# Optimization experiments

Measured on AMD Instinct MI355X. Metric: run time of the kernel, lower is better.

The kernel has to match this reference:

```python
import jax, jax.numpy as jnp
import numpy as np

N = 4096      # num nodes
E = 131072    # num edges
D = 128       # embed dim (in=out)
HID = 16      # kan hidden dim
G, K = 4, 3   # KAN grid_size / spline_order (GCN + FFN kans)
GA, KA = 2, 1 # attention KANLinear grid_size / spline_order
H, HD = 8, 16 # heads, head_dim

def make_grid(in_f, g, k):
    h = 2.0 / g
    pts = (np.arange(-k, g + k + 1) * h - 1.0).astype(np.float32)  # [g+2k+1]
    return jnp.asarray(np.tile(pts[None, :], (in_f, 1)))            # [in_f, g+2k+1]

GRID_D = make_grid(D, G, K)
GRID_H = make_grid(HID, G, K)
GRID_A = make_grid(D, GA, KA)

def b_splines(x, grid, k):
    # x: [n, in] -> B-spline bases [n, in, g+k] via Cox-de-Boor recursion
    x = x[:, :, None]
    g = grid[None]
    bases = ((x >= g[..., :-1]) & (x < g[..., 1:])).astype(x.dtype)
    for j in range(1, k + 1):
        bases = ((x - g[..., :-(j + 1)]) / (g[..., j:-1] - g[..., :-(j + 1)]) * bases[..., :-1]
                 + (g[..., j + 1:] - x) / (g[..., j + 1:] - g[..., 1:-j]) * bases[..., 1:])
    return bases

def kan_lin(x, bw, sw, grid, k, use_silu):
    base = jax.nn.silu(x) if use_silu else x
    return base @ bw.T + jnp.einsum('nig,oig->no', b_splines(x, grid, k), sw)

def ekan2(x, bw1, sw1, bw2, sw2):
    # eKAN with layers_hidden=[D, HID, D], SiLU base activation
    h = kan_lin(x, bw1, sw1, GRID_D, K, True)
    return kan_lin(h, bw2, sw2, GRID_H, K, True)

def layer_norm(h, s, b):
    m = jnp.mean(h, axis=-1, keepdims=True)
    v = jnp.var(h, axis=-1, keepdims=True)
    return (h - m) * jax.lax.rsqrt(v + 1e-5) * s + b

def setup_inputs() -> dict:
    key = jax.random.key(0)
    ks = jax.random.split(key, 20)
    r = lambda i, shape: jax.random.normal(ks[i], shape, jnp.float32) * 0.1
    return dict(
        x=jax.random.normal(ks[0], (N, D), jnp.float32),
        edge_index=jax.random.randint(ks[1], (2, E), 0, N),
        gcn_bw1=r(2, (HID, D)), gcn_sw1=r(3, (HID, D, G + K)),
        gcn_bw2=r(4, (D, HID)), gcn_sw2=r(5, (D, HID, G + K)),
        q_bw=r(6, (D, D)), q_sw=r(7, (D, D, GA + KA)),
        k_bw=r(8, (D, D)), k_sw=r(9, (D, D, GA + KA)),
        v_bw=r(10, (D, D)), v_sw=r(11, (D, D, GA + KA)),
        ffn_bw1=r(12, (HID, D)), ffn_sw1=r(13, (HID, D, G + K)),
        ffn_bw2=r(14, (D, HID)), ffn_sw2=r(15, (D, HID, G + K)),
        ln1_s=jnp.ones(D), ln1_b=jnp.zeros(D),
        ln2_s=jnp.ones(D), ln2_b=jnp.zeros(D),
        ln3_s=jnp.ones(D), ln3_b=jnp.zeros(D),
    )

def reference(x, edge_index, gcn_bw1, gcn_sw1, gcn_bw2, gcn_sw2,
              q_bw, q_sw, k_bw, k_sw, v_bw, v_sw,
              ffn_bw1, ffn_sw1, ffn_bw2, ffn_sw2,
              ln1_s, ln1_b, ln2_s, ln2_b, ln3_s, ln3_b):
    n = x.shape[0]
    # ---- local GCN-KAN branch: KAN(A_hat x) ----
    loops = jnp.arange(n)
    row = jnp.concatenate([edge_index[0], loops])  # sources (+ self-loops)
    col = jnp.concatenate([edge_index[1], loops])  # targets
    w = jnp.ones(row.shape[0], x.dtype)
    deg = jax.ops.segment_sum(w, row, num_segments=n)
    dis = jnp.where(deg > 0, deg ** -0.5, 0.0)
    norm = dis[row] * w * dis[col]
    agg = jax.ops.segment_sum(norm[:, None] * x[row], col, num_segments=n)  # [n, D]
    h_local = ekan2(agg, gcn_bw1, gcn_sw1, gcn_bw2, gcn_sw2)
    h_local = layer_norm(x + h_local, ln1_s, ln1_b)
    # ---- global KAN multi-head attention branch ----
    Q = kan_lin(x, q_bw, q_sw, GRID_A, KA, False).reshape(n, H, HD)
    Kv = kan_lin(x, k_bw, k_sw, GRID_A, KA, False).reshape(n, H, HD)
    V = kan_lin(x, v_bw, v_sw, GRID_A, KA, False).reshape(n, H, HD)
    scores = jnp.einsum('nhd,mhd->hnm', Q, Kv) / np.sqrt(HD)  # [H, n, n]
    attn = jax.nn.softmax(scores, axis=-1)
    h_attn = jnp.einsum('hnm,mhd->nhd', attn, V).reshape(n, D)
    h_attn = layer_norm(x + h_attn, ln2_s, ln2_b)
    # ---- combine + KAN feed-forward ----
    h = h_local + h_attn
    out = layer_norm(h + ekan2(h, ffn_bw1, ffn_sw1, ffn_bw2, ffn_sw2), ln3_s, ln3_b)
    return out
```

## Files before the change

### kernel.cpp

```cpp
#include <hip/hip_runtime.h>

typedef unsigned short u16;
typedef unsigned int u32;

#define D_ 128
#define HID_ 16
#define NH_ 8
#define HD_ 16
#define PSTRIDE 17

#define WE_W1G 0
#define WE_W2G 16384
#define WE_W1F 32768
#define WE_W2F 49152
#define WE_TOTAL 65536

#define KROW 24
#define VROW 136
#define PROW 40
#define HROW 136

#define QSCALE 0.3606737602222409f

typedef __attribute__((ext_vector_type(8))) short bfrag;
typedef __attribute__((ext_vector_type(4))) float ffrag;

#if defined(__has_builtin)
#if __has_builtin(__builtin_amdgcn_exp2f)
#define EXP2F(x) __builtin_amdgcn_exp2f(x)
#endif
#endif
#ifndef EXP2F
#define EXP2F(x) exp2f(x)
#endif


__device__ __forceinline__ float bf2f(u16 u) {
    union { u32 i; float f; } v; v.i = ((u32)u) << 16; return v.f;
}
__device__ __forceinline__ u16 f2bf(float f) {
    u32 x = __float_as_uint(f);
    u32 r = (x + 0x7fffu + ((x >> 16) & 1u)) >> 16;
    return (u16)r;
}
__device__ __forceinline__ float rdf(const void* p, int i, bool bf) {
    return bf ? bf2f(((const u16*)p)[i]) : ((const float*)p)[i];
}

__device__ __forceinline__ u32 probe_stat(const u16* p) {
    for (int i = 0; i < 128; i++) {
        u16 u = p[i];
        int e = (u >> 7) & 0xFF;
        int m = u & 0x7F;
        bool zero = (e == 0) && (m == 0);
        bool sane = zero || (e >= 97 && e <= 147);
        if (!sane) return 0u;
    }
    return 1u;
}

__global__ __launch_bounds__(256) void k_detect(const void* x,
                         const void* gbw1, const void* gsw1, const void* gbw2, const void* gsw2,
                         const void* qbw, const void* qsw, const void* kbw, const void* ksw,
                         const void* vbw, const void* vsw,
                         const void* fbw1, const void* fsw1, const void* fbw2, const void* fsw2,
                         const void* l1s, const void* l1b, const void* l2s, const void* l2b,
                         const void* l3s, const void* l3b,
                         u32* flags, int* __restrict__ cnt3, int N) {
    int t = threadIdx.x;
    const void* ptrs[21] = {x, gbw1, gsw1, gbw2, gsw2, qbw, qsw, kbw, ksw, vbw, vsw,
                            fbw1, fsw1, fbw2, fsw2, l1s, l1b, l2s, l2b, l3s, l3b};
    if (t < 21) {
        u32 f = 0;
        if (t == 15 || t == 17 || t == 19) {
            f = (((const u32*)ptrs[t])[0] != 0x3F800000u) ? 1u : 0u;
        } else if (t == 16 || t == 18 || t == 20) {
            f = 0;
        } else {
            f = probe_stat((const u16*)ptrs[t]);
        }
        flags[t] = f;
    }
    __syncthreads();
    if (t == 16 || t == 18 || t == 20) flags[t] = flags[t - 1];
    int tot = 3 * N;
    for (int i = t; i < tot; i += 256) cnt3[i] = 0;
}

__device__ __forceinline__ float cub_seg(float s) {
    if (s < 0.0f || s >= 4.0f) return 0.0f;
    if (s < 1.0f) return s * s * s * (1.0f / 6.0f);
    if (s < 2.0f) { float r = s - 1.0f; return (1.0f + 3.0f * r + 3.0f * r * r - 3.0f * r * r * r) * (1.0f / 6.0f); }
    if (s < 3.0f) { float r = s - 2.0f; return (4.0f - 6.0f * r * r + 3.0f * r * r * r) * (1.0f / 6.0f); }
    float q = 4.0f - s; return q * q * q * (1.0f / 6.0f);
}
__device__ __forceinline__ float lin_seg(float s) {
    if (s < 0.0f || s >= 2.0f) return 0.0f;
    return (s < 1.0f) ? s : (2.0f - s);
}

__device__ __forceinline__ float bsum(float v, float* tmp) {
#pragma unroll
    for (int off = 1; off < 64; off <<= 1) v += __shfl_xor(v, off, 64);
    __syncthreads();
    if ((threadIdx.x & 63) == 0) tmp[threadIdx.x >> 6] = v;
    __syncthreads();
    return tmp[0] + tmp[1];
}

__device__ __forceinline__ uint4 feat8(float a) {
    float si = a / (1.0f + __expf(-a));
    float u = (a + 2.5f) * 2.0f;
    float b0 = cub_seg(u), b1 = cub_seg(u - 1.0f), b2 = cub_seg(u - 2.0f), b3 = cub_seg(u - 3.0f);
    float b4 = cub_seg(u - 4.0f), b5 = cub_seg(u - 5.0f), b6 = cub_seg(u - 6.0f);
    uint4 r;
    r.x = (u32)f2bf(si) | ((u32)f2bf(b0) << 16);
    r.y = (u32)f2bf(b1) | ((u32)f2bf(b2) << 16);
    r.z = (u32)f2bf(b3) | ((u32)f2bf(b4) << 16);
    r.w = (u32)f2bf(b5) | ((u32)f2bf(b6) << 16);
    return r;
}

__global__ __launch_bounds__(256) void k_setup(const void* __restrict__ x,
        const void* l1s, const void* l1b, const void* l2s,
        const void* l2b, const void* l3s, const void* l3b,
        const void* gbw1, const void* gsw1, const void* gbw2, const void* gsw2,
        const void* fbw1, const void* fsw1, const void* fbw2, const void* fsw2,
        const void* qbw, const void* qsw, const void* kbw, const void* ksw,
        const void* vbw, const void* vsw,
        const int* __restrict__ ei,
        const u32* __restrict__ flags,
        float* __restrict__ xin, float* __restrict__ lnp,
        u16* __restrict__ F,
        u16* __restrict__ Web, u16* __restrict__ Wb,
        int* __restrict__ cnt, int* __restrict__ degi,
        int N, int E) {
    int b = blockIdx.x;
    int convB = ((N * D_ + 768) + 255) >> 8;
    if (b < convB) {
        int i = b * 256 + threadIdx.x;
        if (i < N * D_) {
            float xv = rdf(x, i, flags[0] != 0);
            xin[i] = xv;
            float u = xv + 2.0f;
            u32 lo = (u32)f2bf(xv) | ((u32)f2bf(lin_seg(u)) << 16);
            u32 hi = (u32)f2bf(lin_seg(u - 1.0f)) | ((u32)f2bf(lin_seg(u - 2.0f)) << 16);
            ((uint2*)F)[i] = make_uint2(lo, hi);
        } else if (i < N * D_ + 768) {
            int j = i - N * D_;
            int sel = j >> 7, k = j & 127;
            const void* p = sel == 0 ? l1s : sel == 1 ? l1b : sel == 2 ? l2s
                         : sel == 3 ? l2b : sel == 4 ? l3s : l3b;
            lnp[j] = rdf(p, k, flags[15 + sel] != 0);
        }
    } else if (b < convB + 224) {
        int t = (b - convB) * 256 + threadIdx.x;
        if (t < 8192) {
            int seg = t >> 11, i = t & 2047;
            const void* bw = seg == 0 ? gbw1 : seg == 1 ? gbw2 : seg == 2 ? fbw1 : fbw2;
            const void* sw = seg == 0 ? gsw1 : seg == 1 ? gsw2 : seg == 2 ? fsw1 : fsw2;
            int fb = seg == 0 ? 1 : seg == 1 ? 3 : seg == 2 ? 11 : 13;
            bool bwbf = flags[fb] != 0, swbf = flags[fb + 1] != 0;
            u16* dst = Web + (size_t)seg * 16384 + (size_t)i * 8;
            dst[0] = f2bf(rdf(bw, i, bwbf));
#pragma unroll
            for (int g = 0; g < 7; g++) dst[1 + g] = f2bf(rdf(sw, i * 7 + g, swbf));
        } else if (t < 8192 + 49152) {
            int uu = t - 8192;
            int seg = uu >> 14, i = uu & 16383;
            const void* bw = seg == 0 ? qbw : seg == 1 ? kbw : vbw;
            const void* sw = seg == 0 ? qsw : seg == 1 ? ksw : vsw;
            int fb = 5 + seg * 2;
            bool bwbf = flags[fb] != 0, swbf = flags[fb + 1] != 0;
            float sc = (seg == 0) ? QSCALE : 1.0f;
            u16* dst = Wb + (size_t)seg * 65536 + (size_t)i * 4;
            dst[0] = f2bf(rdf(bw, i, bwbf) * sc);
#pragma unroll
            for (int g = 0; g < 3; g++) dst[1 + g] = f2bf(rdf(sw, i * 3 + g, swbf) * sc);
        }
    } else {
        int e = (b - convB - 224) * 256 + threadIdx.x;
        if (e < E) {
            atomicAdd(&degi[ei[e]], 1);
            atomicAdd(&cnt[ei[E + e]], 1);
        }
    }
}

__global__ __launch_bounds__(1024) void k_scan(const int* __restrict__ cnt,
                                               const int* __restrict__ degi,
                                               int* __restrict__ rowptr,
                                               float* __restrict__ dis, int N) {
    __shared__ int ws[16];
    int t = threadIdx.x;
    int base = t * 4;
    int a[4];
#pragma unroll
    for (int k = 0; k < 4; k++) a[k] = (base + k < N) ? cnt[base + k] : 0;
    int loc = a[0] + a[1] + a[2] + a[3];
    int pre = loc;
#pragma unroll
    for (int off = 1; off < 64; off <<= 1) {
        int v = __shfl_up(pre, off, 64);
        if ((t & 63) >= off) pre += v;
    }
    if ((t & 63) == 63) ws[t >> 6] = pre;
    __syncthreads();
    if (t < 64) {
        int v = (t < 16) ? ws[t] : 0;
#pragma unroll
        for (int off = 1; off < 16; off <<= 1) {
            int u = __shfl_up(v, off, 64);
            if (t >= off) v += u;
        }
        if (t < 16) ws[t] = v;
    }
    __syncthreads();
    int ex = pre - loc + ((t >= 64) ? ws[(t >> 6) - 1] : 0);
    int run = ex;
#pragma unroll
    for (int k = 0; k < 4; k++) {
        if (base + k < N) rowptr[base + k] = run;
        run += a[k];
    }
    if (t == 1023) rowptr[N] = ws[15];
#pragma unroll
    for (int k = 0; k < 4; k++)
        if (base + k < N) dis[base + k] = rsqrtf((float)degi[base + k] + 1.0f);
}

__global__ void k_fill(const int* __restrict__ ei, const int* __restrict__ rowptr,
                       int* __restrict__ fill, int* __restrict__ elist, int E) {
    int e = blockIdx.x * 256 + threadIdx.x;
    if (e < E) {
        int r = ei[e], c = ei[E + e];
        int pos = rowptr[c] + atomicAdd(&fill[c], 1);
        elist[pos] = r;
    }
}

__global__ __launch_bounds__(128) void k_gcn(const int* __restrict__ rowptr,
        const int* __restrict__ elist, const float* __restrict__ dis,
        const float* __restrict__ xin, u16* __restrict__ Afeat) {
    int c = blockIdx.x, t = threadIdx.x;
    __shared__ int ids[128];
    __shared__ float wsh[128];
    int beg = rowptr[c], end = rowptr[c + 1];
    float acc = 0.0f, acc2 = 0.0f;
    for (int j0 = beg; j0 < end; j0 += 128) {
        int cc = min(128, end - j0);
        __syncthreads();
        if (t < cc) {
            int rr = elist[j0 + t];
            ids[t] = rr;
            wsh[t] = dis[rr];
        }
        __syncthreads();
        int j = 0;
        for (; j + 2 <= cc; j += 2) {
            acc  += wsh[j]     * xin[(size_t)ids[j] * D_ + t];
            acc2 += wsh[j + 1] * xin[(size_t)ids[j + 1] * D_ + t];
        }
        if (j < cc) acc += wsh[j] * xin[(size_t)ids[j] * D_ + t];
    }
    float dc = dis[c];
    float a = dc * (acc + acc2 + dc * xin[(size_t)c * D_ + t]);
    ((uint4*)Afeat)[(size_t)c * D_ + t] = feat8(a);
}

__global__ __launch_bounds__(64) void k_ekan_mm(const u16* __restrict__ A,
        const u16* __restrict__ W1b, const u16* __restrict__ W2b,
        const float* __restrict__ resid,
        const float* __restrict__ lns, const float* __restrict__ lnb,
        void* __restrict__ outp, const u32* __restrict__ flags, int fin, int N) {
    __shared__ u16 hfL[16 * HROW];
    int mt = blockIdx.x;
    int lane = threadIdx.x, quad = lane >> 4, l15 = lane & 15;
    const u16* ar = A + (size_t)(mt * 16 + l15) * 1024 + quad * 8;
    const u16* br = W1b + (size_t)l15 * 1024 + quad * 8;
    ffrag acc = {0, 0, 0, 0};
#pragma unroll
    for (int ks = 0; ks < 1024; ks += 32) {
        bfrag af = *(const bfrag*)(ar + ks);
        bfrag bf = *(const bfrag*)(br + ks);
        acc = __builtin_amdgcn_mfma_f32_16x16x32_bf16(af, bf, acc, 0, 0, 0);
    }
#define G1EPI(RR, COMP) { \
    uint4 fv = feat8(acc.COMP); \
    *(uint4*)(&hfL[(quad * 4 + RR) * HROW + l15 * 8]) = fv; }
    G1EPI(0, x) G1EPI(1, y) G1EPI(2, z) G1EPI(3, w)
#undef G1EPI
    __asm__ volatile("s_waitcnt lgkmcnt(0)" ::: "memory");
    __builtin_amdgcn_wave_barrier();
    const u16* b0 = W2b + (size_t)l15 * 128 + quad * 8;
    ffrag a0 = {0,0,0,0}, a1 = {0,0,0,0}, a2 = {0,0,0,0}, a3 = {0,0,0,0};
    ffrag a4 = {0,0,0,0}, a5 = {0,0,0,0}, a6 = {0,0,0,0}, a7 = {0,0,0,0};
#pragma unroll
    for (int ks = 0; ks < 128; ks += 32) {
        bfrag af = *(const bfrag*)(&hfL[l15 * HROW + quad * 8 + ks]);
        a0 = __builtin_amdgcn_mfma_f32_16x16x32_bf16(af, *(const bfrag*)(b0 + 0 * 2048 + ks), a0, 0, 0, 0);
        a1 = __builtin_amdgcn_mfma_f32_16x16x32_bf16(af, *(const bfrag*)(b0 + 1 * 2048 + ks), a1, 0, 0, 0);
        a2 = __builtin_amdgcn_mfma_f32_16x16x32_bf16(af, *(const bfrag*)(b0 + 2 * 2048 + ks), a2, 0, 0, 0);
        a3 = __builtin_amdgcn_mfma_f32_16x16x32_bf16(af, *(const bfrag*)(b0 + 3 * 2048 + ks), a3, 0, 0, 0);
        a4 = __builtin_amdgcn_mfma_f32_16x16x32_bf16(af, *(const bfrag*)(b0 + 4 * 2048 + ks), a4, 0, 0, 0);
        a5 = __builtin_amdgcn_mfma_f32_16x16x32_bf16(af, *(const bfrag*)(b0 + 5 * 2048 + ks), a5, 0, 0, 0);
        a6 = __builtin_amdgcn_mfma_f32_16x16x32_bf16(af, *(const bfrag*)(b0 + 6 * 2048 + ks), a6, 0, 0, 0);
        a7 = __builtin_amdgcn_mfma_f32_16x16x32_bf16(af, *(const bfrag*)(b0 + 7 * 2048 + ks), a7, 0, 0, 0);
    }
    float ls0 = lns[l15],       lb0 = lnb[l15];
    float ls1 = lns[16 + l15],  lb1 = lnb[16 + l15];
    float ls2 = lns[32 + l15],  lb2 = lnb[32 + l15];
    float ls3 = lns[48 + l15],  lb3 = lnb[48 + l15];
    float ls4 = lns[64 + l15],  lb4 = lnb[64 + l15];
    float ls5 = lns[80 + l15],  lb5 = lnb[80 + l15];
    float ls6 = lns[96 + l15],  lb6 = lnb[96 + l15];
    float ls7 = lns[112 + l15], lb7 = lnb[112 + l15];
    bool bfo = (fin != 0) && (flags[0] != 0);
#define G2EPI(RR, COMP) { \
    int node = mt * 16 + quad * 4 + RR; \
    const float* rr_ = resid + (size_t)node * 128 + l15; \
    float v0 = a0.COMP + rr_[0];   float v1 = a1.COMP + rr_[16]; \
    float v2 = a2.COMP + rr_[32];  float v3 = a3.COMP + rr_[48]; \
    float v4 = a4.COMP + rr_[64];  float v5 = a5.COMP + rr_[80]; \
    float v6 = a6.COMP + rr_[96];  float v7 = a7.COMP + rr_[112]; \
    float s1 = ((v0 + v1) + (v2 + v3)) + ((v4 + v5) + (v6 + v7)); \
    float s2 = ((v0*v0 + v1*v1) + (v2*v2 + v3*v3)) + ((v4*v4 + v5*v5) + (v6*v6 + v7*v7)); \
    s1 += __shfl_xor(s1, 1, 64); s2 += __shfl_xor(s2, 1, 64); \
    s1 += __shfl_xor(s1, 2, 64); s2 += __shfl_xor(s2, 2, 64); \
    s1 += __shfl_xor(s1, 4, 64); s2 += __shfl_xor(s2, 4, 64); \
    s1 += __shfl_xor(s1, 8, 64); s2 += __shfl_xor(s2, 8, 64); \
    float mean = s1 * 0.0078125f; \
    float var = s2 * 0.0078125f - mean * mean; \
    float rs = rsqrtf(var + 1e-5f); \
    float y0 = (v0 - mean) * rs * ls0 + lb0; float y1 = (v1 - mean) * rs * ls1 + lb1; \
    float y2 = (v2 - mean) * rs * ls2 + lb2; float y3 = (v3 - mean) * rs * ls3 + lb3; \
    float y4 = (v4 - mean) * rs * ls4 + lb4; float y5 = (v5 - mean) * rs * ls5 + lb5; \
    float y6 = (v6 - mean) * rs * ls6 + lb6; float y7 = (v7 - mean) * rs * ls7 + lb7; \
    if (bfo) { \
        u16* ob = (u16*)outp + (size_t)node * 128 + l15; \
        ob[0] = f2bf(y0); ob[16] = f2bf(y1); ob[32] = f2bf(y2); ob[48] = f2bf(y3); \
        ob[64] = f2bf(y4); ob[80] = f2bf(y5); ob[96] = f2bf(y6); ob[112] = f2bf(y7); \
    } else { \
        float* ob = (float*)outp + (size_t)node * 128 + l15; \
        ob[0] = y0; ob[16] = y1; ob[32] = y2; ob[48] = y3; \
        ob[64] = y4; ob[80] = y5; ob[96] = y6; ob[112] = y7; \
    } }
    G2EPI(0, x) G2EPI(1, y) G2EPI(2, z) G2EPI(3, w)
#undef G2EPI
}

#define QKV_STORE(ACC, TL) { \
    int col = cg * 48 + (TL) * 16 + l15; \
    int mat = col >> 7, idx = col & 127; \
    u16* dstb = (mat == 0) ? Qb : (mat == 1) ? Kb : Vb; \
    size_t base = (size_t)(idx >> 4) * N * HD_ + (size_t)(idx & 15); \
    dstb[base + (size_t)(rowb + 0) * HD_] = f2bf(ACC.x); \
    dstb[base + (size_t)(rowb + 1) * HD_] = f2bf(ACC.y); \
    dstb[base + (size_t)(rowb + 2) * HD_] = f2bf(ACC.z); \
    dstb[base + (size_t)(rowb + 3) * HD_] = f2bf(ACC.w); \
}

__global__ __launch_bounds__(64) void k_qkv5(const u16* __restrict__ F,
        const u16* __restrict__ Wb,
        u16* __restrict__ Qb, u16* __restrict__ Kb, u16* __restrict__ Vb, int N) {
    int mt = blockIdx.x, cg = blockIdx.y;
    int lane = threadIdx.x, quad = lane >> 4, l15 = lane & 15;
    const u16* arow = F + (size_t)(mt * 16 + l15) * 512 + quad * 8;
    const u16* b0r = Wb + (size_t)(cg * 48 + l15) * 512 + quad * 8;
    const u16* b1r = b0r + 16 * 512;
    const u16* b2r = b0r + 32 * 512;
    ffrag a0 = {0, 0, 0, 0}, a1 = {0, 0, 0, 0}, a2 = {0, 0, 0, 0};
#pragma unroll
    for (int ks = 0; ks < 512; ks += 32) {
        bfrag af = *(const bfrag*)(arow + ks);
        bfrag bf0 = *(const bfrag*)(b0r + ks);
        bfrag bf1 = *(const bfrag*)(b1r + ks);
        bfrag bf2 = *(const bfrag*)(b2r + ks);
        a0 = __builtin_amdgcn_mfma_f32_16x16x32_bf16(af, bf0, a0, 0, 0, 0);
        a1 = __builtin_amdgcn_mfma_f32_16x16x32_bf16(af, bf1, a1, 0, 0, 0);
        a2 = __builtin_amdgcn_mfma_f32_16x16x32_bf16(af, bf2, a2, 0, 0, 0);
    }
    int rowb = mt * 16 + quad * 4;
    QKV_STORE(a0, 0)
    QKV_STORE(a1, 1)
    QKV_STORE(a2, 2)
}

#define ATTN_SCORE(QF, LACC, PBT) { \
    ffrag zz = {0.0f, 0.0f, 0.0f, 0.0f}; \
    ffrag s0 = __builtin_amdgcn_mfma_f32_16x16x32_bf16(QF, kf0, zz, 0, 0, 0); \
    ffrag s1 = __builtin_amdgcn_mfma_f32_16x16x32_bf16(QF, kf1, zz, 0, 0, 0); \
    float a0 = EXP2F(s0.x), a1 = EXP2F(s0.y), a2 = EXP2F(s0.z), a3 = EXP2F(s0.w); \
    float b0 = EXP2F(s1.x), b1 = EXP2F(s1.y), b2 = EXP2F(s1.z), b3 = EXP2F(s1.w); \
    LACC.x += a0 + b0; LACC.y += a1 + b1; LACC.z += a2 + b2; LACC.w += a3 + b3; \
    u32* pw = (u32*)PBT; \
    pw[(quad * 4 + 0) * (PROW / 2) + l15] = (__float_as_uint(a0) >> 16) | (__float_as_uint(b0) & 0xFFFF0000u); \
    pw[(quad * 4 + 1) * (PROW / 2) + l15] = (__float_as_uint(a1) >> 16) | (__float_as_uint(b1) & 0xFFFF0000u); \
    pw[(quad * 4 + 2) * (PROW / 2) + l15] = (__float_as_uint(a2) >> 16) | (__float_as_uint(b2) & 0xFFFF0000u); \
    pw[(quad * 4 + 3) * (PROW / 2) + l15] = (__float_as_uint(a3) >> 16) | (__float_as_uint(b3) & 0xFFFF0000u); \
}

#define ATTN_PV(OACC, PBT) { \
    bfrag pf = *(const bfrag*)(&PBT[l15 * PROW + quad * 8]); \
    OACC = __builtin_amdgcn_mfma_f32_16x16x32_bf16(pf, vf, OACC, 0, 0, 0); \
}

#define STORE_TILE(OACC, LACC, TL) { \
    int q0 = qtb + (TL) * 16 + quad * 4; \
    float* pp; \
    pp = part + ((size_t)(h * N + q0 + 0) * SPLIT + s) * PSTRIDE; \
    pp[1 + l15] = OACC.x; if (l15 == 0) pp[0] = LACC.x; \
    pp = part + ((size_t)(h * N + q0 + 1) * SPLIT + s) * PSTRIDE; \
    pp[1 + l15] = OACC.y; if (l15 == 0) pp[0] = LACC.y; \
    pp = part + ((size_t)(h * N + q0 + 2) * SPLIT + s) * PSTRIDE; \
    pp[1 + l15] = OACC.z; if (l15 == 0) pp[0] = LACC.z; \
    pp = part + ((size_t)(h * N + q0 + 3) * SPLIT + s) * PSTRIDE; \
    pp[1 + l15] = OACC.w; if (l15 == 0) pp[0] = LACC.w; \
}

__global__ __launch_bounds__(256) void k_attn9(const u16* __restrict__ Qb,
        const u16* __restrict__ Kb, const u16* __restrict__ Vb,
        float* __restrict__ part, int N, int SPLIT) {
    int s = blockIdx.x, qb = blockIdx.y, h = blockIdx.z;
    int t = threadIdx.x;
    int w = t >> 6, lane = t & 63, quad = lane >> 4, l15 = lane & 15;
    __shared__ u16 ldsK[128 * KROW + 16];
    __shared__ u16 ldsVt[16 * VROW];
    __shared__ u16 ldsP[4][4][16 * PROW];

    const u16* qrow = Qb + (size_t)h * N * HD_;
    const u16* krow = Kb + (size_t)h * N * HD_;
    const u16* vrow = Vb + (size_t)h * N * HD_;

    for (int i = t; i < (128 * KROW + 16) / 2; i += 256) ((u32*)ldsK)[i] = 0;

    int qtb = qb * 256 + w * 64;
    bfrag qz = {0, 0, 0, 0, 0, 0, 0, 0};
    bfrag qf0 = qz, qf1 = qz, qf2 = qz, qf3 = qz;
    if (quad < 2) {
        qf0 = *(const bfrag*)(qrow + (size_t)(qtb + 0 * 16 + l15) * HD_ + quad * 8);
        qf1 = *(const bfrag*)(qrow + (size_t)(qtb + 1 * 16 + l15) * HD_ + quad * 8);
        qf2 = *(const bfrag*)(qrow + (size_t)(qtb + 2 * 16 + l15) * HD_ + quad * 8);
        qf3 = *(const bfrag*)(qrow + (size_t)(qtb + 3 * 16 + l15) * HD_ + quad * 8);
    }

    ffrag o0 = {0, 0, 0, 0}, o1 = {0, 0, 0, 0}, o2 = {0, 0, 0, 0}, o3 = {0, 0, 0, 0};
    ffrag L0 = {0, 0, 0, 0}, L1 = {0, 0, 0, 0}, L2 = {0, 0, 0, 0}, L3 = {0, 0, 0, 0};
    u16* pb0 = &ldsP[w][0][0];
    u16* pb1 = &ldsP[w][1][0];
    u16* pb2 = &ldsP[w][2][0];
    u16* pb3 = &ldsP[w][3][0];

    int keys = N / SPLIT;
    int kstart0 = s * keys;
    for (int kst = 0; kst < keys; kst += 128) {
        int kg = kstart0 + kst;
        __syncthreads();
        if (t < 128) {
            const uint4* src = (const uint4*)(krow + (size_t)(kg + t) * HD_);
            uint4 a = src[0], b = src[1];
            *(uint4*)(&ldsK[t * KROW]) = a;
            *(uint4*)(&ldsK[t * KROW + 8]) = b;
        } else {
            int key = t - 128;
            const uint4* src = (const uint4*)(vrow + (size_t)(kg + key) * HD_);
            uint4 a = src[0], b = src[1];
            ldsVt[0 * VROW + key] = (u16)(a.x);  ldsVt[1 * VROW + key] = (u16)(a.x >> 16);
            ldsVt[2 * VROW + key] = (u16)(a.y);  ldsVt[3 * VROW + key] = (u16)(a.y >> 16);
            ldsVt[4 * VROW + key] = (u16)(a.z);  ldsVt[5 * VROW + key] = (u16)(a.z >> 16);
            ldsVt[6 * VROW + key] = (u16)(a.w);  ldsVt[7 * VROW + key] = (u16)(a.w >> 16);
            ldsVt[8 * VROW + key] = (u16)(b.x);  ldsVt[9 * VROW + key] = (u16)(b.x >> 16);
            ldsVt[10 * VROW + key] = (u16)(b.y); ldsVt[11 * VROW + key] = (u16)(b.y >> 16);
            ldsVt[12 * VROW + key] = (u16)(b.z); ldsVt[13 * VROW + key] = (u16)(b.z >> 16);
            ldsVt[14 * VROW + key] = (u16)(b.w); ldsVt[15 * VROW + key] = (u16)(b.w >> 16);
        }
        __syncthreads();
#pragma unroll
        for (int koff = 0; koff < 128; koff += 32) {
            bfrag kf0 = *(const bfrag*)(&ldsK[(koff + 2 * l15) * KROW + quad * 8]);
            bfrag kf1 = *(const bfrag*)(&ldsK[(koff + 2 * l15 + 1) * KROW + quad * 8]);
            bfrag vf = *(const bfrag*)(&ldsVt[l15 * VROW + koff + quad * 8]);
            ATTN_SCORE(qf0, L0, pb0)
            ATTN_SCORE(qf1, L1, pb1)
            ATTN_SCORE(qf2, L2, pb2)
            ATTN_SCORE(qf3, L3, pb3)
            __asm__ volatile("s_waitcnt lgkmcnt(0)" ::: "memory");
            ATTN_PV(o0, pb0)
            ATTN_PV(o1, pb1)
            ATTN_PV(o2, pb2)
            ATTN_PV(o3, pb3)
        }
    }

#pragma unroll
    for (int off = 1; off < 16; off <<= 1) {
        L0.x += __shfl_xor(L0.x, off, 64); L0.y += __shfl_xor(L0.y, off, 64);
        L0.z += __shfl_xor(L0.z, off, 64); L0.w += __shfl_xor(L0.w, off, 64);
        L1.x += __shfl_xor(L1.x, off, 64); L1.y += __shfl_xor(L1.y, off, 64);
        L1.z += __shfl_xor(L1.z, off, 64); L1.w += __shfl_xor(L1.w, off, 64);
        L2.x += __shfl_xor(L2.x, off, 64); L2.y += __shfl_xor(L2.y, off, 64);
        L2.z += __shfl_xor(L2.z, off, 64); L2.w += __shfl_xor(L2.w, off, 64);
        L3.x += __shfl_xor(L3.x, off, 64); L3.y += __shfl_xor(L3.y, off, 64);
        L3.z += __shfl_xor(L3.z, off, 64); L3.w += __shfl_xor(L3.w, off, 64);
    }
    STORE_TILE(o0, L0, 0)
    STORE_TILE(o1, L1, 1)
    STORE_TILE(o2, L2, 2)
    STORE_TILE(o3, L3, 3)
}

__global__ __launch_bounds__(128) void k_comb(const float* __restrict__ part,
        const float* __restrict__ xin, const float* __restrict__ hl,
        const float* __restrict__ lnp, float* __restrict__ hv,
        u16* __restrict__ Afeat, int N, int SPLIT) {
    int n = blockIdx.x, t = threadIdx.x;
    __shared__ float red[128];
    int h = t >> 4, d = t & 15;
    float L = 0.0f, O = 0.0f;
    for (int ss = 0; ss < SPLIT; ss++) {
        const float* ps = part + ((size_t)(h * N + n) * SPLIT + ss) * PSTRIDE;
        L += ps[0];
        O += ps[1 + d];
    }
    float ha = O / L;
    float r = xin[(size_t)n * D_ + t] + ha;
    float mean = bsum(r, red) * (1.0f / 128.0f);
    float c = r - mean;
    float var = bsum(c * c, red) * (1.0f / 128.0f);
    float y2 = c * rsqrtf(var + 1e-5f) * lnp[256 + t] + lnp[384 + t];
    float hvv = hl[(size_t)n * D_ + t] + y2;
    hv[(size_t)n * D_ + t] = hvv;
    ((uint4*)Afeat)[(size_t)n * D_ + t] = feat8(hvv);
}

extern "C" void kernel_launch(void* const* d_in, const int* in_sizes, int n_in,
                              void* d_out, int out_size, void* d_ws, size_t ws_size,
                              hipStream_t stream) {
    const void* x = d_in[0];
    const int* ei = (const int*)d_in[1];
    const void* gbw1 = d_in[2];
    const void* gsw1 = d_in[3];
    const void* gbw2 = d_in[4];
    const void* gsw2 = d_in[5];
    const void* qbw = d_in[6];
    const void* qsw = d_in[7];
    const void* kbw = d_in[8];
    const void* ksw = d_in[9];
    const void* vbw = d_in[10];
    const void* vsw = d_in[11];
    const void* fbw1 = d_in[12];
    const void* fsw1 = d_in[13];
    const void* fbw2 = d_in[14];
    const void* fsw2 = d_in[15];
    const void* ln1s = d_in[16];
    const void* ln1b = d_in[17];
    const void* ln2s = d_in[18];
    const void* ln2b = d_in[19];
    const void* ln3s = d_in[20];
    const void* ln3b = d_in[21];

    const int N = in_sizes[0] / D_;
    const int E = in_sizes[1] / 2;
    const size_t ND = (size_t)N * D_;

    float* wf = (float*)d_ws;
    u32* flags = (u32*)wf;
    float* lnp = wf + 32;
    float* dis = wf + 800;
    float* xin = dis + N;
    float* hl  = xin + ND;
    float* hv  = hl + ND;
    u16* Web = (u16*)(hv + ND);
    u16* Wb  = Web + WE_TOTAL;
    u16* F   = Wb + 196608;
    u16* Qb  = F + (size_t)N * 512;
    u16* Kb  = Qb + ND;
    u16* Vb  = Kb + ND;
    u16* Afeat = Vb + ND;
    int* cnt    = (int*)(Afeat + (size_t)N * 1024);
    int* fill   = cnt + N;
    int* degi   = fill + N;
    int* rowptr = degi + N;
    int* elist  = rowptr + N + 1;
    float* part = (float*)(elist + E);

    size_t baseBytes = (size_t)((char*)part - (char*)d_ws);
    int SPLIT = 8;
    if (baseBytes + (size_t)NH_ * N * 8 * PSTRIDE * 4 > ws_size) SPLIT = 4;
    if (baseBytes + (size_t)NH_ * N * 4 * PSTRIDE * 4 > ws_size) SPLIT = 2;

    int convB = ((N * D_ + 768) + 255) >> 8;
    int countB = (E + 255) / 256;

    k_detect<<<1, 256, 0, stream>>>(x, gbw1, gsw1, gbw2, gsw2, qbw, qsw, kbw, ksw,
                                    vbw, vsw, fbw1, fsw1, fbw2, fsw2,
                                    ln1s, ln1b, ln2s, ln2b, ln3s, ln3b, flags, cnt, N);
    k_setup<<<convB + 224 + countB, 256, 0, stream>>>(
        x, ln1s, ln1b, ln2s, ln2b, ln3s, ln3b,
        gbw1, gsw1, gbw2, gsw2, fbw1, fsw1, fbw2, fsw2,
        qbw, qsw, kbw, ksw, vbw, vsw,
        ei, flags, xin, lnp, F, Web, Wb, cnt, degi, N, E);
    k_scan<<<1, 1024, 0, stream>>>(cnt, degi, rowptr, dis, N);
    k_fill<<<countB, 256, 0, stream>>>(ei, rowptr, fill, elist, E);
    k_gcn<<<N, 128, 0, stream>>>(rowptr, elist, dis, xin, Afeat);
    k_ekan_mm<<<N / 16, 64, 0, stream>>>(Afeat, Web + WE_W1G, Web + WE_W2G, xin,
                                         lnp + 0, lnp + 128, hl, flags, 0, N);
    k_qkv5<<<dim3(N / 16, 8), 64, 0, stream>>>(F, Wb, Qb, Kb, Vb, N);
    k_attn9<<<dim3(SPLIT, N / 256, NH_), 256, 0, stream>>>(Qb, Kb, Vb, part, N, SPLIT);
    k_comb<<<N, 128, 0, stream>>>(part, xin, hl, lnp, hv, Afeat, N, SPLIT);
    k_ekan_mm<<<N / 16, 64, 0, stream>>>(Afeat, Web + WE_W1F, Web + WE_W2F, hv,
                                         lnp + 512, lnp + 640, d_out, flags, 1, N);
}
```

Measured before the change: 241.7 us.

## Fuse GCN aggregation and combine stages with eKAN matmuls via shared-memory features

```diff
diff --git a/kernel.cpp b/kernel.cpp
--- a/kernel.cpp
+++ b/kernel.cpp
@@ -19,6 +19,8 @@
 #define VROW 136
 #define PROW 40
 #define HROW 136
+#define AROW 1032
+#define HVROW 132
 
 #define QSCALE 0.3606737602222409f
 
@@ -97,15 +99,6 @@
 __device__ __forceinline__ float lin_seg(float s) {
     if (s < 0.0f || s >= 2.0f) return 0.0f;
     return (s < 1.0f) ? s : (2.0f - s);
-}
-
-__device__ __forceinline__ float bsum(float v, float* tmp) {
-#pragma unroll
-    for (int off = 1; off < 64; off <<= 1) v += __shfl_xor(v, off, 64);
-    __syncthreads();
-    if ((threadIdx.x & 63) == 0) tmp[threadIdx.x >> 6] = v;
-    __syncthreads();
-    return tmp[0] + tmp[1];
 }
 
 __device__ __forceinline__ uint4 feat8(float a) {
@@ -239,114 +232,135 @@
     }
 }
 
-__global__ __launch_bounds__(128) void k_gcn(const int* __restrict__ rowptr,
-        const int* __restrict__ elist, const float* __restrict__ dis,
-        const float* __restrict__ xin, u16* __restrict__ Afeat) {
-    int c = blockIdx.x, t = threadIdx.x;
-    __shared__ int ids[128];
-    __shared__ float wsh[128];
-    int beg = rowptr[c], end = rowptr[c + 1];
-    float acc = 0.0f, acc2 = 0.0f;
-    for (int j0 = beg; j0 < end; j0 += 128) {
-        int cc = min(128, end - j0);
-        __syncthreads();
-        if (t < cc) {
-            int rr = elist[j0 + t];
-            ids[t] = rr;
-            wsh[t] = dis[rr];
-        }
-        __syncthreads();
-        int j = 0;
-        for (; j + 2 <= cc; j += 2) {
-            acc  += wsh[j]     * xin[(size_t)ids[j] * D_ + t];
-            acc2 += wsh[j + 1] * xin[(size_t)ids[j + 1] * D_ + t];
-        }
-        if (j < cc) acc += wsh[j] * xin[(size_t)ids[j] * D_ + t];
-    }
-    float dc = dis[c];
-    float a = dc * (acc + acc2 + dc * xin[(size_t)c * D_ + t]);
-    ((uint4*)Afeat)[(size_t)c * D_ + t] = feat8(a);
-}
-
-__global__ __launch_bounds__(64) void k_ekan_mm(const u16* __restrict__ A,
-        const u16* __restrict__ W1b, const u16* __restrict__ W2b,
-        const float* __restrict__ resid,
-        const float* __restrict__ lns, const float* __restrict__ lnb,
-        void* __restrict__ outp, const u32* __restrict__ flags, int fin, int N) {
-    __shared__ u16 hfL[16 * HROW];
-    int mt = blockIdx.x;
-    int lane = threadIdx.x, quad = lane >> 4, l15 = lane & 15;
-    const u16* ar = A + (size_t)(mt * 16 + l15) * 1024 + quad * 8;
-    const u16* br = W1b + (size_t)l15 * 1024 + quad * 8;
-    ffrag acc = {0, 0, 0, 0};
-#pragma unroll
-    for (int ks = 0; ks < 1024; ks += 32) {
-        bfrag af = *(const bfrag*)(ar + ks);
-        bfrag bf = *(const bfrag*)(br + ks);
-        acc = __builtin_amdgcn_mfma_f32_16x16x32_bf16(af, bf, acc, 0, 0, 0);
-    }
-#define G1EPI(RR, COMP) { \
-    uint4 fv = feat8(acc.COMP); \
-    *(uint4*)(&hfL[(quad * 4 + RR) * HROW + l15 * 8]) = fv; }
-    G1EPI(0, x) G1EPI(1, y) G1EPI(2, z) G1EPI(3, w)
-#undef G1EPI
-    __asm__ volatile("s_waitcnt lgkmcnt(0)" ::: "memory");
-    __builtin_amdgcn_wave_barrier();
-    const u16* b0 = W2b + (size_t)l15 * 128 + quad * 8;
-    ffrag a0 = {0,0,0,0}, a1 = {0,0,0,0}, a2 = {0,0,0,0}, a3 = {0,0,0,0};
-    ffrag a4 = {0,0,0,0}, a5 = {0,0,0,0}, a6 = {0,0,0,0}, a7 = {0,0,0,0};
-#pragma unroll
-    for (int ks = 0; ks < 128; ks += 32) {
-        bfrag af = *(const bfrag*)(&hfL[l15 * HROW + quad * 8 + ks]);
-        a0 = __builtin_amdgcn_mfma_f32_16x16x32_bf16(af, *(const bfrag*)(b0 + 0 * 2048 + ks), a0, 0, 0, 0);
-        a1 = __builtin_amdgcn_mfma_f32_16x16x32_bf16(af, *(const bfrag*)(b0 + 1 * 2048 + ks), a1, 0, 0, 0);
-        a2 = __builtin_amdgcn_mfma_f32_16x16x32_bf16(af, *(const bfrag*)(b0 + 2 * 2048 + ks), a2, 0, 0, 0);
-        a3 = __builtin_amdgcn_mfma_f32_16x16x32_bf16(af, *(const bfrag*)(b0 + 3 * 2048 + ks), a3, 0, 0, 0);
-        a4 = __builtin_amdgcn_mfma_f32_16x16x32_bf16(af, *(const bfrag*)(b0 + 4 * 2048 + ks), a4, 0, 0, 0);
-        a5 = __builtin_amdgcn_mfma_f32_16x16x32_bf16(af, *(const bfrag*)(b0 + 5 * 2048 + ks), a5, 0, 0, 0);
-        a6 = __builtin_amdgcn_mfma_f32_16x16x32_bf16(af, *(const bfrag*)(b0 + 6 * 2048 + ks), a6, 0, 0, 0);
-        a7 = __builtin_amdgcn_mfma_f32_16x16x32_bf16(af, *(const bfrag*)(b0 + 7 * 2048 + ks), a7, 0, 0, 0);
-    }
-    float ls0 = lns[l15],       lb0 = lnb[l15];
-    float ls1 = lns[16 + l15],  lb1 = lnb[16 + l15];
-    float ls2 = lns[32 + l15],  lb2 = lnb[32 + l15];
-    float ls3 = lns[48 + l15],  lb3 = lnb[48 + l15];
-    float ls4 = lns[64 + l15],  lb4 = lnb[64 + l15];
-    float ls5 = lns[80 + l15],  lb5 = lnb[80 + l15];
-    float ls6 = lns[96 + l15],  lb6 = lnb[96 + l15];
-    float ls7 = lns[112 + l15], lb7 = lnb[112 + l15];
-    bool bfo = (fin != 0) && (flags[0] != 0);
-#define G2EPI(RR, COMP) { \
-    int node = mt * 16 + quad * 4 + RR; \
-    const float* rr_ = resid + (size_t)node * 128 + l15; \
-    float v0 = a0.COMP + rr_[0];   float v1 = a1.COMP + rr_[16]; \
-    float v2 = a2.COMP + rr_[32];  float v3 = a3.COMP + rr_[48]; \
-    float v4 = a4.COMP + rr_[64];  float v5 = a5.COMP + rr_[80]; \
-    float v6 = a6.COMP + rr_[96];  float v7 = a7.COMP + rr_[112]; \
-    float s1 = ((v0 + v1) + (v2 + v3)) + ((v4 + v5) + (v6 + v7)); \
-    float s2 = ((v0*v0 + v1*v1) + (v2*v2 + v3*v3)) + ((v4*v4 + v5*v5) + (v6*v6 + v7*v7)); \
+#define EKAN_G1(W1B) \
+    if (ww == 0) { \
+        const u16* ar = hfA + (size_t)l15 * AROW + quad * 8; \
+        const u16* br = (W1B) + (size_t)l15 * 1024 + quad * 8; \
+        ffrag c0 = {0,0,0,0}, c1 = {0,0,0,0}, c2 = {0,0,0,0}, c3 = {0,0,0,0}; \
+        for (int ks = 0; ks < 256; ks += 32) { \
+            c0 = __builtin_amdgcn_mfma_f32_16x16x32_bf16(*(const bfrag*)(ar + ks),       *(const bfrag*)(br + ks),       c0, 0, 0, 0); \
+            c1 = __builtin_amdgcn_mfma_f32_16x16x32_bf16(*(const bfrag*)(ar + 256 + ks), *(const bfrag*)(br + 256 + ks), c1, 0, 0, 0); \
+            c2 = __builtin_amdgcn_mfma_f32_16x16x32_bf16(*(const bfrag*)(ar + 512 + ks), *(const bfrag*)(br + 512 + ks), c2, 0, 0, 0); \
+            c3 = __builtin_amdgcn_mfma_f32_16x16x32_bf16(*(const bfrag*)(ar + 768 + ks), *(const bfrag*)(br + 768 + ks), c3, 0, 0, 0); \
+        } \
+        float e0 = (c0.x + c1.x) + (c2.x + c3.x); \
+        float e1 = (c0.y + c1.y) + (c2.y + c3.y); \
+        float e2 = (c0.z + c1.z) + (c2.z + c3.z); \
+        float e3 = (c0.w + c1.w) + (c2.w + c3.w); \
+        { uint4 fv = feat8(e0); *(uint4*)(&hfL[(quad * 4 + 0) * HROW + l15 * 8]) = fv; } \
+        { uint4 fv = feat8(e1); *(uint4*)(&hfL[(quad * 4 + 1) * HROW + l15 * 8]) = fv; } \
+        { uint4 fv = feat8(e2); *(uint4*)(&hfL[(quad * 4 + 2) * HROW + l15 * 8]) = fv; } \
+        { uint4 fv = feat8(e3); *(uint4*)(&hfL[(quad * 4 + 3) * HROW + l15 * 8]) = fv; } \
+    }
+
+#define EK_TGET(RR, COMP, V0, V1, RES0EXPR, RES1EXPR) { \
+    int row = quad * 4 + RR; \
+    float r0 = (RES0EXPR); \
+    float r1 = (RES1EXPR); \
+    V0 = a0.COMP + r0; V1 = a1.COMP + r1; \
+    float s1 = V0 + V1, s2 = V0 * V0 + V1 * V1; \
     s1 += __shfl_xor(s1, 1, 64); s2 += __shfl_xor(s2, 1, 64); \
     s1 += __shfl_xor(s1, 2, 64); s2 += __shfl_xor(s2, 2, 64); \
     s1 += __shfl_xor(s1, 4, 64); s2 += __shfl_xor(s2, 4, 64); \
     s1 += __shfl_xor(s1, 8, 64); s2 += __shfl_xor(s2, 8, 64); \
+    if (l15 == 0) { redS[ww * 16 + row] = s1; redS[64 + ww * 16 + row] = s2; } }
+
+#define EK_TOUT(RR, V0, V1, OUTP, BFO) { \
+    int row = quad * 4 + RR; \
+    float s1 = (redS[row] + redS[16 + row]) + (redS[32 + row] + redS[48 + row]); \
+    float s2 = (redS[64 + row] + redS[80 + row]) + (redS[96 + row] + redS[112 + row]); \
     float mean = s1 * 0.0078125f; \
     float var = s2 * 0.0078125f - mean * mean; \
     float rs = rsqrtf(var + 1e-5f); \
-    float y0 = (v0 - mean) * rs * ls0 + lb0; float y1 = (v1 - mean) * rs * ls1 + lb1; \
-    float y2 = (v2 - mean) * rs * ls2 + lb2; float y3 = (v3 - mean) * rs * ls3 + lb3; \
-    float y4 = (v4 - mean) * rs * ls4 + lb4; float y5 = (v5 - mean) * rs * ls5 + lb5; \
-    float y6 = (v6 - mean) * rs * ls6 + lb6; float y7 = (v7 - mean) * rs * ls7 + lb7; \
-    if (bfo) { \
-        u16* ob = (u16*)outp + (size_t)node * 128 + l15; \
-        ob[0] = f2bf(y0); ob[16] = f2bf(y1); ob[32] = f2bf(y2); ob[48] = f2bf(y3); \
-        ob[64] = f2bf(y4); ob[80] = f2bf(y5); ob[96] = f2bf(y6); ob[112] = f2bf(y7); \
+    float y0 = (V0 - mean) * rs * ls0 + lb0; \
+    float y1 = (V1 - mean) * rs * ls1 + lb1; \
+    int node = node0 + row; \
+    if (BFO) { \
+        u16* ob = (u16*)(OUTP) + (size_t)node * 128; \
+        ob[c0i] = f2bf(y0); ob[c1i] = f2bf(y1); \
     } else { \
-        float* ob = (float*)outp + (size_t)node * 128 + l15; \
-        ob[0] = y0; ob[16] = y1; ob[32] = y2; ob[48] = y3; \
-        ob[64] = y4; ob[80] = y5; ob[96] = y6; ob[112] = y7; \
+        float* ob = (float*)(OUTP) + (size_t)node * 128; \
+        ob[c0i] = y0; ob[c1i] = y1; \
     } }
-    G2EPI(0, x) G2EPI(1, y) G2EPI(2, z) G2EPI(3, w)
-#undef G2EPI
+
+#define EKAN_G2LN(W2B, LNS, LNB, RES0EXPR, RES1EXPR, OUTP, BFO) { \
+    const u16* b0 = (W2B) + (size_t)l15 * 128 + quad * 8 + (size_t)(2 * ww) * 2048; \
+    ffrag a0 = {0,0,0,0}, a1 = {0,0,0,0}; \
+    for (int ks = 0; ks < 128; ks += 32) { \
+        bfrag af = *(const bfrag*)(&hfL[l15 * HROW + quad * 8 + ks]); \
+        a0 = __builtin_amdgcn_mfma_f32_16x16x32_bf16(af, *(const bfrag*)(b0 + ks),        a0, 0, 0, 0); \
+        a1 = __builtin_amdgcn_mfma_f32_16x16x32_bf16(af, *(const bfrag*)(b0 + 2048 + ks), a1, 0, 0, 0); \
+    } \
+    int c0i = 32 * ww + l15, c1i = c0i + 16; \
+    float ls0 = (LNS)[c0i], lb0 = (LNB)[c0i]; \
+    float ls1 = (LNS)[c1i], lb1 = (LNB)[c1i]; \
+    float v0r0, v0r1, v0r2, v0r3, v1r0, v1r1, v1r2, v1r3; \
+    EK_TGET(0, x, v0r0, v1r0, RES0EXPR, RES1EXPR) \
+    EK_TGET(1, y, v0r1, v1r1, RES0EXPR, RES1EXPR) \
+    EK_TGET(2, z, v0r2, v1r2, RES0EXPR, RES1EXPR) \
+    EK_TGET(3, w, v0r3, v1r3, RES0EXPR, RES1EXPR) \
+    __syncthreads(); \
+    EK_TOUT(0, v0r0, v1r0, OUTP, BFO) \
+    EK_TOUT(1, v0r1, v1r1, OUTP, BFO) \
+    EK_TOUT(2, v0r2, v1r2, OUTP, BFO) \
+    EK_TOUT(3, v0r3, v1r3, OUTP, BFO) }
+
+__global__ __launch_bounds__(256) void k_gcn_ekan(
+        const int* __restrict__ rowptr, const int* __restrict__ elist,
+        const float* __restrict__ dis, const float* __restrict__ xin,
+        const u16* __restrict__ W1b, const u16* __restrict__ W2b,
+        const float* __restrict__ lns, const float* __restrict__ lnb,
+        float* __restrict__ hl, int N) {
+    __shared__ u16 hfA[16 * AROW];
+    __shared__ u16 hfL[16 * HROW];
+    __shared__ float redS[128];
+    __shared__ int idsH[2][128];
+    __shared__ float wshH[2][128];
+    int mt = blockIdx.x, t = threadIdx.x;
+    int half = t >> 7, d = t & 127;
+    int ww = t >> 6, lane = t & 63, quad = lane >> 4, l15 = lane & 15;
+    int node0 = mt * 16;
+#pragma unroll 1
+    for (int i = 0; i < 16; i += 2) {
+        int nodeA = node0 + i, nodeB = node0 + i + 1;
+        int begA = rowptr[nodeA], endA = rowptr[nodeA + 1];
+        int begB = rowptr[nodeB], endB = rowptr[nodeB + 1];
+        int tripsA = (endA - begA + 127) >> 7;
+        int tripsB = (endB - begB + 127) >> 7;
+        int trips = max(tripsA, tripsB);
+        int beg = half ? begB : begA;
+        int end = half ? endB : endA;
+        float acc = 0.0f, acc2 = 0.0f;
+        for (int tr = 0; tr < trips; tr++) {
+            int j0 = beg + (tr << 7);
+            int cc = min(128, end - j0);
+            __syncthreads();
+            if (d < cc) {
+                int rr = elist[j0 + d];
+                idsH[half][d] = rr;
+                wshH[half][d] = dis[rr];
+            }
+            __syncthreads();
+            int j = 0;
+            for (; j + 2 <= cc; j += 2) {
+                acc  += wshH[half][j]     * xin[(size_t)idsH[half][j]     * D_ + d];
+                acc2 += wshH[half][j + 1] * xin[(size_t)idsH[half][j + 1] * D_ + d];
+            }
+            if (j < cc) acc += wshH[half][j] * xin[(size_t)idsH[half][j] * D_ + d];
+        }
+        int node = half ? nodeB : nodeA;
+        float dc = dis[node];
+        float a = dc * (acc + acc2 + dc * xin[(size_t)node * D_ + d]);
+        *(uint4*)(&hfA[(i + half) * AROW + d * 8]) = feat8(a);
+    }
+    __syncthreads();
+    EKAN_G1(W1b)
+    __syncthreads();
+    EKAN_G2LN(W2b, lns, lnb,
+              xin[(size_t)(node0 + row) * 128 + c0i],
+              xin[(size_t)(node0 + row) * 128 + c1i],
+              hl, false)
+    (void)lane;
 }
 
 #define QKV_STORE(ACC, TL) { \
@@ -509,28 +523,60 @@
     STORE_TILE(o3, L3, 3)
 }
 
-__global__ __launch_bounds__(128) void k_comb(const float* __restrict__ part,
+__global__ __launch_bounds__(256) void k_comb_ekan(
+        const float* __restrict__ part,
         const float* __restrict__ xin, const float* __restrict__ hl,
-        const float* __restrict__ lnp, float* __restrict__ hv,
-        u16* __restrict__ Afeat, int N, int SPLIT) {
-    int n = blockIdx.x, t = threadIdx.x;
-    __shared__ float red[128];
-    int h = t >> 4, d = t & 15;
-    float L = 0.0f, O = 0.0f;
-    for (int ss = 0; ss < SPLIT; ss++) {
-        const float* ps = part + ((size_t)(h * N + n) * SPLIT + ss) * PSTRIDE;
-        L += ps[0];
-        O += ps[1 + d];
-    }
-    float ha = O / L;
-    float r = xin[(size_t)n * D_ + t] + ha;
-    float mean = bsum(r, red) * (1.0f / 128.0f);
-    float c = r - mean;
-    float var = bsum(c * c, red) * (1.0f / 128.0f);
-    float y2 = c * rsqrtf(var + 1e-5f) * lnp[256 + t] + lnp[384 + t];
-    float hvv = hl[(size_t)n * D_ + t] + y2;
-    hv[(size_t)n * D_ + t] = hvv;
-    ((uint4*)Afeat)[(size_t)n * D_ + t] = feat8(hvv);
+        const float* __restrict__ lnp,
+        const u16* __restrict__ W1b, const u16* __restrict__ W2b,
+        void* __restrict__ outp, const u32* __restrict__ flags,
+        int N, int SPLIT) {
+    __shared__ u16 hfA[16 * AROW];
+    __shared__ u16 hfL[16 * HROW];
+    __shared__ float redS[128];
+    __shared__ float hvL[16 * HVROW];
+    __shared__ float redA[4], redB[4];
+    int mt = blockIdx.x, t = threadIdx.x;
+    int half = t >> 7, tl = t & 127;
+    int ww = t >> 6, lane = t & 63, quad = lane >> 4, l15 = lane & 15;
+    int hh = tl >> 4, dd = tl & 15;
+    int node0 = mt * 16;
+#pragma unroll 1
+    for (int i = 0; i < 16; i += 2) {
+        int node = node0 + i + half;
+        float L = 0.0f, O = 0.0f;
+        for (int ss = 0; ss < SPLIT; ss++) {
+            const float* ps = part + ((size_t)(hh * N + node) * SPLIT + ss) * PSTRIDE;
+            L += ps[0];
+            O += ps[1 + dd];
+        }
+        float r = xin[(size_t)node * D_ + tl] + O / L;
+        float s1 = r, s2 = r * r;
+#pragma unroll
+        for (int off = 1; off < 64; off <<= 1) {
+            s1 += __shfl_xor(s1, off, 64);
+            s2 += __shfl_xor(s2, off, 64);
+        }
+        if ((t & 63) == 0) { redA[ww] = s1; redB[ww] = s2; }
+        __syncthreads();
+        float S1 = redA[half * 2] + redA[half * 2 + 1];
+        float S2 = redB[half * 2] + redB[half * 2 + 1];
+        float mean = S1 * 0.0078125f;
+        float var = S2 * 0.0078125f - mean * mean;
+        float rs = rsqrtf(var + 1e-5f);
+        float y2 = (r - mean) * rs * lnp[256 + tl] + lnp[384 + tl];
+        float hvv = hl[(size_t)node * D_ + tl] + y2;
+        hvL[(i + half) * HVROW + tl] = hvv;
+        *(uint4*)(&hfA[(i + half) * AROW + tl * 8]) = feat8(hvv);
+        __syncthreads();
+    }
+    bool bfo = flags[0] != 0;
+    EKAN_G1(W1b)
+    __syncthreads();
+    EKAN_G2LN(W2b, lnp + 512, lnp + 640,
+              hvL[row * HVROW + c0i],
+              hvL[row * HVROW + c1i],
+              outp, bfo)
+    (void)lane;
 }
 
 extern "C" void kernel_launch(void* const* d_in, const int* in_sizes, int n_in,
@@ -569,15 +615,13 @@
     float* dis = wf + 800;
     float* xin = dis + N;
     float* hl  = xin + ND;
-    float* hv  = hl + ND;
-    u16* Web = (u16*)(hv + ND);
+    u16* Web = (u16*)(hl + ND);
     u16* Wb  = Web + WE_TOTAL;
     u16* F   = Wb + 196608;
     u16* Qb  = F + (size_t)N * 512;
     u16* Kb  = Qb + ND;
     u16* Vb  = Kb + ND;
-    u16* Afeat = Vb + ND;
-    int* cnt    = (int*)(Afeat + (size_t)N * 1024);
+    int* cnt    = (int*)(Vb + ND);
     int* fill   = cnt + N;
     int* degi   = fill + N;
     int* rowptr = degi + N;
@@ -600,14 +644,14 @@
         gbw1, gsw1, gbw2, gsw2, fbw1, fsw1, fbw2, fsw2,
         qbw, qsw, kbw, ksw, vbw, vsw,
         ei, flags, xin, lnp, F, Web, Wb, cnt, degi, N, E);
+    k_qkv5<<<dim3(N / 16, 8), 64, 0, stream>>>(F, Wb, Qb, Kb, Vb, N);
     k_scan<<<1, 1024, 0, stream>>>(cnt, degi, rowptr, dis, N);
     k_fill<<<countB, 256, 0, stream>>>(ei, rowptr, fill, elist, E);
-    k_gcn<<<N, 128, 0, stream>>>(rowptr, elist, dis, xin, Afeat);
-    k_ekan_mm<<<N / 16, 64, 0, stream>>>(Afeat, Web + WE_W1G, Web + WE_W2G, xin,
-                                         lnp + 0, lnp + 128, hl, flags, 0, N);
-    k_qkv5<<<dim3(N / 16, 8), 64, 0, stream>>>(F, Wb, Qb, Kb, Vb, N);
+    k_gcn_ekan<<<N / 16, 256, 0, stream>>>(rowptr, elist, dis, xin,
+                                           Web + WE_W1G, Web + WE_W2G,
+                                           lnp + 0, lnp + 128, hl, N);
     k_attn9<<<dim3(SPLIT, N / 256, NH_), 256, 0, stream>>>(Qb, Kb, Vb, part, N, SPLIT);
-    k_comb<<<N, 128, 0, stream>>>(part, xin, hl, lnp, hv, Afeat, N, SPLIT);
-    k_ekan_mm<<<N / 16, 64, 0, stream>>>(Afeat, Web + WE_W1F, Web + WE_W2F, hv,
-                                         lnp + 512, lnp + 640, d_out, flags, 1, N);
-}
+    k_comb_ekan<<<N / 16, 256, 0, stream>>>(part, xin, hl, lnp,
+                                            Web + WE_W1F, Web + WE_W2F,
+                                            d_out, flags, N, SPLIT);
+}
```

Result: slower. 283.5 us (+17.3%).
